# Kernel tuning notes

Hardware: AMD Instinct MI355X
Metric: run time of the kernel (lower is better)

The kernel has to match this reference:

```python
import jax, jax.numpy as jnp
import numpy as np

K_DIM = 256
HEADS = 8


def setup_inputs() -> dict:
    key = jax.random.key(0)
    ks = jax.random.split(key, 6)
    b, t, k, h = 8, 1024, K_DIM, HEADS
    scale = 1.0 / np.sqrt(k)
    x = jax.random.normal(ks[0], (b, t, k), dtype=jnp.float32)
    # nn.Linear(k, k*h, bias=False) weights, stored as (in, out) for x @ W
    Wq = jax.random.normal(ks[1], (k, k * h), dtype=jnp.float32) * scale
    Wk = jax.random.normal(ks[2], (k, k * h), dtype=jnp.float32) * scale
    Wv = jax.random.normal(ks[3], (k, k * h), dtype=jnp.float32) * scale
    # unifyheads: nn.Linear(h*k, k) with bias
    Wu = jax.random.normal(ks[4], (h * k, k), dtype=jnp.float32) * (1.0 / np.sqrt(h * k))
    bu = jax.random.normal(ks[5], (k,), dtype=jnp.float32) * 0.01
    return {"x": x, "Wq": Wq, "Wk": Wk, "Wv": Wv, "Wu": Wu, "bu": bu}


def reference(x, Wq, Wk, Wv, Wu, bu):
    b, t, k = x.shape
    h = Wq.shape[1] // k
    inv4 = 1.0 / (k ** 0.25)  # scale Q and K each by k^(1/4) -> combined 1/sqrt(k)
    q = (x @ Wq).reshape(b, t, h, k) * inv4
    kk = (x @ Wk).reshape(b, t, h, k) * inv4
    v = (x @ Wv).reshape(b, t, h, k)
    # scores: [b, h, t, t]
    scores = jnp.einsum('bthk,bshk->bhts', q, kk)
    att = jax.nn.softmax(scores, axis=-1)
    out = jnp.einsum('bhts,bshk->bthk', att, v).reshape(b, t, h * k)
    return out @ Wu + bu
```

## Files before the change

kernel.cpp:

```cpp
#include <hip/hip_runtime.h>
#include <stdint.h>

typedef unsigned short u16;
typedef __attribute__((ext_vector_type(8))) short bf16x8;
typedef __attribute__((ext_vector_type(4))) float f32x4;

#define LOG2E 1.44269504088896340736f

__device__ __forceinline__ float bf2f(u16 u) {
  union { uint32_t u; float f; } v; v.u = ((uint32_t)u) << 16; return v.f;
}
__device__ __forceinline__ u16 f2bf(float f) {
  union { float f; uint32_t u; } v; v.f = f;
  uint32_t r = v.u + 0x7fffu + ((v.u >> 16) & 1u);
  return (u16)(r >> 16);
}

__device__ __forceinline__ void gl_lds16(const u16* g, u16* l) {
  __builtin_amdgcn_global_load_lds((const __attribute__((address_space(1))) void*)g,
                                   (__attribute__((address_space(3))) void*)l, 16, 0, 0);
}

__global__ __launch_bounds__(256) void k_cvt_x(const float* __restrict__ x,
                                               u16* __restrict__ xb) {
  const int i = blockIdx.x * 256 + threadIdx.x;
  float4 v = ((const float4*)x)[i];
  ushort4 o;
  o.x = f2bf(v.x); o.y = f2bf(v.y); o.z = f2bf(v.z); o.w = f2bf(v.w);
  ((ushort4*)xb)[i] = o;
}

__device__ __forceinline__ void transpose64f(const float* src, int sstride,
                                             u16* dst, int dstride,
                                             float scale, u16* tile ) {
  const int tid = threadIdx.x;
  const int row = tid >> 3, seg = tid & 7;
#pragma unroll
  for (int p = 0; p < 2; ++p) {
    int rr = p * 32 + row;
    int rw = rr ^ (seg * 8);
    float4 a = *(const float4*)(src + rr * sstride + seg * 8);
    float4 b = *(const float4*)(src + rr * sstride + seg * 8 + 4);
    tile[(seg * 8 + 0) * 80 + rw] = f2bf(a.x * scale);
    tile[(seg * 8 + 1) * 80 + rw] = f2bf(a.y * scale);
    tile[(seg * 8 + 2) * 80 + rw] = f2bf(a.z * scale);
    tile[(seg * 8 + 3) * 80 + rw] = f2bf(a.w * scale);
    tile[(seg * 8 + 4) * 80 + rw] = f2bf(b.x * scale);
    tile[(seg * 8 + 5) * 80 + rw] = f2bf(b.y * scale);
    tile[(seg * 8 + 6) * 80 + rw] = f2bf(b.z * scale);
    tile[(seg * 8 + 7) * 80 + rw] = f2bf(b.w * scale);
  }
  __syncthreads();
#pragma unroll
  for (int p = 0; p < 2; ++p) {
    int rr = p * 32 + row;
    int sw = (seg ^ ((rr >> 3) & 7)) * 8;
    *(uint4*)(dst + rr * dstride + seg * 8) = *(uint4*)(tile + rr * 80 + sw);
  }
}

__device__ __forceinline__ void transpose64(const u16* src, int sstride,
                                            u16* dst, int dstride, u16* tile) {
  const int tid = threadIdx.x;
  const int row = tid >> 3, seg = tid & 7;
  union { uint4 u; u16 s[8]; } tv;
#pragma unroll
  for (int p = 0; p < 2; ++p) {
    int rr = p * 32 + row;
    int rw = rr ^ (seg * 8);
    tv.u = *(const uint4*)(src + rr * sstride + seg * 8);
#pragma unroll
    for (int j = 0; j < 8; ++j)
      tile[(seg * 8 + j) * 80 + rw] = tv.s[j];
  }
  __syncthreads();
#pragma unroll
  for (int p = 0; p < 2; ++p) {
    int rr = p * 32 + row;
    int sw = (seg ^ ((rr >> 3) & 7)) * 8;
    *(uint4*)(dst + rr * dstride + seg * 8) = *(uint4*)(tile + rr * 80 + sw);
  }
}

__global__ __launch_bounds__(256) void k_transpose_wqkv(const float* __restrict__ Wq,
                                                        const float* __restrict__ Wk,
                                                        const float* __restrict__ Wv,
                                                        u16* __restrict__ Wt) {
  __shared__ u16 tile[64 * 80];
  const int o0 = blockIdx.x * 64, i0 = blockIdx.y * 64;
  const float* src; float scale = 0.25f; int oc0 = o0;
  if (o0 < 2048)      { src = Wq; }
  else if (o0 < 4096) { src = Wk; oc0 = o0 - 2048; }
  else                { src = Wv; oc0 = o0 - 4096; scale = 1.0f; }
  transpose64f(src + i0 * 2048 + oc0, 2048, Wt + o0 * 256 + i0, 256, scale, tile);
}

__global__ __launch_bounds__(256) void k_transpose_wu(const float* __restrict__ Wu,
                                                      u16* __restrict__ Wut) {
  __shared__ u16 tile[64 * 80];
  const int c0 = blockIdx.x * 64, r0 = blockIdx.y * 64;
  transpose64f(Wu + r0 * 256 + c0, 256, Wut + c0 * 2048 + r0, 2048, 1.0f, tile);
}

__global__ __launch_bounds__(256) void k_transpose_v(const u16* __restrict__ qkv,
                                                     u16* __restrict__ vt) {
  __shared__ u16 tile[64 * 80];
  const int bh = blockIdx.z;
  const int b = bh >> 3, h = bh & 7;
  const int t0 = blockIdx.y * 64, d0 = blockIdx.x * 64;
  const u16* src = qkv + ((size_t)(b * 1024 + t0)) * 6144 + 4096 + h * 256 + d0;
  u16* dst = vt + ((size_t)(bh * 256 + d0)) * 1024 + t0;
  transpose64(src, 6144, dst, 1024, tile);
}

__global__ __launch_bounds__(256) void k_gemm_qkv(const u16* __restrict__ A,
                                                  const u16* __restrict__ Bt,
                                                  u16* __restrict__ C) {
  __shared__ u16 As[128 * 32];
  __shared__ u16 Bs[128 * 32];
  const int m0 = blockIdx.y * 128, n0 = blockIdx.x * 128;
  const int tid = threadIdx.x, w = tid >> 6, lane = tid & 63;
  const int q = lane >> 4, r = lane & 15;
  const int wm = (w >> 1) * 64, wn = (w & 1) * 64;
  const int bo0 = w * 2048 + lane * 16;
  const int row0 = bo0 >> 6, col0 = (bo0 & 63) >> 1;
  const int bo1 = bo0 + 1024;
  const int row1 = bo1 >> 6, col1 = (bo1 & 63) >> 1;
  f32x4 acc[4][4] = {};
  for (int kt = 0; kt < 256; kt += 32) {
    __syncthreads();
    gl_lds16(A + (m0 + row0) * 256 + kt + col0, As + w * 1024);
    gl_lds16(A + (m0 + row1) * 256 + kt + col1, As + w * 1024 + 512);
    gl_lds16(Bt + (n0 + row0) * 256 + kt + col0, Bs + w * 1024);
    gl_lds16(Bt + (n0 + row1) * 256 + kt + col1, Bs + w * 1024 + 512);
    __syncthreads();
    bf16x8 af[4], bf[4];
#pragma unroll
    for (int mb = 0; mb < 4; ++mb) af[mb] = *(const bf16x8*)(As + (wm + mb * 16 + r) * 32 + q * 8);
#pragma unroll
    for (int nb = 0; nb < 4; ++nb) bf[nb] = *(const bf16x8*)(Bs + (wn + nb * 16 + r) * 32 + q * 8);
#pragma unroll
    for (int mb = 0; mb < 4; ++mb)
#pragma unroll
      for (int nb = 0; nb < 4; ++nb)
        acc[mb][nb] = __builtin_amdgcn_mfma_f32_16x16x32_bf16(af[mb], bf[nb], acc[mb][nb], 0, 0, 0);
  }
#pragma unroll
  for (int mb = 0; mb < 4; ++mb)
#pragma unroll
    for (int nb = 0; nb < 4; ++nb) {
      const int nn = n0 + wn + nb * 16 + r;
#pragma unroll
      for (int reg = 0; reg < 4; ++reg) {
        const int mm = m0 + wm + mb * 16 + q * 4 + reg;
        C[(size_t)mm * 6144 + nn] = f2bf(acc[mb][nb][reg]);
      }
    }
}

__global__ __launch_bounds__(256, 2) void k_attn(const u16* __restrict__ qkv,
                                                 const u16* __restrict__ vt,
                                                 u16* __restrict__ att) {
  __shared__ u16 smem[17152];
  const int blk = blockIdx.x;
  const int qt = blk >> 6, bh = blk & 63;
  const int b = bh >> 3, h = bh & 7;
  const int tid = threadIdx.x, w = tid >> 6, lane = tid & 63;
  const int q = lane >> 4, r = lane & 15;
  const int t0 = qt * 128 + w * 32;

  const u16* QgA = qkv + ((size_t)(b * 1024 + t0 + r)) * 6144 + h * 256;
  const u16* QgB = QgA + (size_t)16 * 6144;
  bf16x8 qfA[8], qfB[8];
#pragma unroll
  for (int kc = 0; kc < 8; ++kc) {
    qfA[kc] = *(const bf16x8*)(QgA + kc * 32 + q * 8);
    qfB[kc] = *(const bf16x8*)(QgB + kc * 32 + q * 8);
  }

  float lA = 0.0f, lB = 0.0f;
  f32x4 oA[16] = {}, oB[16] = {};

  const u16* Kg = qkv + (size_t)b * 1024 * 6144 + 2048 + h * 256;
  const u16* Vg = vt + (size_t)(b * 8 + h) * 256 * 1024;

  const int kc_s = (tid & 31) >> 2, kq_s = tid & 3;
  const int db_s = tid >> 4, vr_s = tid & 15;

  for (int sc = 0; sc < 1024; sc += 32) {
    __syncthreads();
    {
      uint4 kv[4];
#pragma unroll
      for (int p = 0; p < 4; ++p) {
        int key = p * 8 + (tid >> 5);
        kv[p] = *(const uint4*)(Kg + (size_t)(sc + key) * 6144 + (tid & 31) * 8);
      }
#pragma unroll
      for (int p = 0; p < 4; ++p) {
        int key = p * 8 + (tid >> 5);
        int sb = key >> 4, kr = key & 15;
        int unit = (kc_s * 2 + sb) * 64 + kq_s * 16 + ((kr + kq_s + kc_s * 4) & 15);
        *(uint4*)(smem + unit * 8) = kv[p];
      }
    }
    {
      uint4 vv[4];
#pragma unroll
      for (int p = 0; p < 4; ++p)
        vv[p] = *(const uint4*)(Vg + (size_t)tid * 1024 + sc + p * 8);
#pragma unroll
      for (int p = 0; p < 4; ++p) {
        int unit = db_s * 64 + p * 16 + ((vr_s + p) & 15);
        *(uint4*)(smem + 8192 + unit * 8) = vv[p];
      }
    }
    __syncthreads();

    f32x4 s0A = {}, s1A = {}, s0B = {}, s1B = {};
#pragma unroll
    for (int kc = 0; kc < 8; ++kc) {
      bf16x8 k0 = *(const bf16x8*)(smem + ((kc * 2 + 0) * 64 + q * 16 + ((r + q + kc * 4) & 15)) * 8);
      bf16x8 k1 = *(const bf16x8*)(smem + ((kc * 2 + 1) * 64 + q * 16 + ((r + q + kc * 4) & 15)) * 8);
      s0A = __builtin_amdgcn_mfma_f32_16x16x32_bf16(k0, qfA[kc], s0A, 0, 0, 0);
      s1A = __builtin_amdgcn_mfma_f32_16x16x32_bf16(k1, qfA[kc], s1A, 0, 0, 0);
      s0B = __builtin_amdgcn_mfma_f32_16x16x32_bf16(k0, qfB[kc], s0B, 0, 0, 0);
      s1B = __builtin_amdgcn_mfma_f32_16x16x32_bf16(k1, qfB[kc], s1B, 0, 0, 0);
    }

    union { bf16x8 v; u16 e[8]; } pfA, pfB;
    {
      float pa[4], pb[4];
#pragma unroll
      for (int reg = 0; reg < 4; ++reg) {
        pa[reg] = exp2f(s0A[reg] * LOG2E);
        pb[reg] = exp2f(s1A[reg] * LOG2E);
        lA += pa[reg] + pb[reg];
      }
      uint32_t pk[4];
#pragma unroll
      for (int reg = 0; reg < 4; ++reg)
        pk[reg] = (uint32_t)f2bf(pa[reg]) | ((uint32_t)f2bf(pb[reg]) << 16);
      const int srcA = ((q & 1) << 5) + r, srcB = srcA + 16;
      uint32_t tt[8];
#pragma unroll
      for (int reg = 0; reg < 4; ++reg) tt[reg] = (uint32_t)__shfl((int)pk[reg], srcA);
#pragma unroll
      for (int reg = 0; reg < 4; ++reg) tt[4 + reg] = (uint32_t)__shfl((int)pk[reg], srcB);
      const bool hi = (q >= 2);
#pragma unroll
      for (int j = 0; j < 8; ++j)
        pfA.e[j] = hi ? (u16)(tt[j] >> 16) : (u16)(tt[j] & 0xffffu);
    }
    {
      float pa[4], pb[4];
#pragma unroll
      for (int reg = 0; reg < 4; ++reg) {
        pa[reg] = exp2f(s0B[reg] * LOG2E);
        pb[reg] = exp2f(s1B[reg] * LOG2E);
        lB += pa[reg] + pb[reg];
      }
      uint32_t pk[4];
#pragma unroll
      for (int reg = 0; reg < 4; ++reg)
        pk[reg] = (uint32_t)f2bf(pa[reg]) | ((uint32_t)f2bf(pb[reg]) << 16);
      const int srcA = ((q & 1) << 5) + r, srcB = srcA + 16;
      uint32_t tt[8];
#pragma unroll
      for (int reg = 0; reg < 4; ++reg) tt[reg] = (uint32_t)__shfl((int)pk[reg], srcA);
#pragma unroll
      for (int reg = 0; reg < 4; ++reg) tt[4 + reg] = (uint32_t)__shfl((int)pk[reg], srcB);
      const bool hi = (q >= 2);
#pragma unroll
      for (int j = 0; j < 8; ++j)
        pfB.e[j] = hi ? (u16)(tt[j] >> 16) : (u16)(tt[j] & 0xffffu);
    }

#pragma unroll
    for (int db = 0; db < 16; ++db) {
      bf16x8 vf = *(const bf16x8*)(smem + 8192 + (db * 64 + q * 16 + ((r + q) & 15)) * 8);
      oA[db] = __builtin_amdgcn_mfma_f32_16x16x32_bf16(vf, pfA.v, oA[db], 0, 0, 0);
      oB[db] = __builtin_amdgcn_mfma_f32_16x16x32_bf16(vf, pfB.v, oB[db], 0, 0, 0);
    }
  }

  lA += __shfl_xor(lA, 16); lA += __shfl_xor(lA, 32);
  lB += __shfl_xor(lB, 16); lB += __shfl_xor(lB, 32);
  float rlA = 1.0f / lA, rlB = 1.0f / lB;

  __syncthreads();
  u16* Os = smem + w * 4288;
#pragma unroll
  for (int pass = 0; pass < 2; ++pass) {
    const f32x4* o = pass ? oB : oA;
    const float rl = pass ? rlB : rlA;
    const int tb = t0 + pass * 16;
    __syncthreads();
#pragma unroll
    for (int db = 0; db < 16; ++db) {
      uint32_t lo = (uint32_t)f2bf(o[db][0] * rl) | ((uint32_t)f2bf(o[db][1] * rl) << 16);
      uint32_t hi2 = (uint32_t)f2bf(o[db][2] * rl) | ((uint32_t)f2bf(o[db][3] * rl) << 16);
      uint2 val; val.x = lo; val.y = hi2;
      *(uint2*)(Os + r * 268 + db * 16 + q * 4) = val;
    }
    asm volatile("s_waitcnt lgkmcnt(0)" ::: "memory");
    u16* Ag = att + ((size_t)(b * 1024 + tb)) * 2048 + h * 256;
#pragma unroll
    for (int p = 0; p < 8; ++p) {
      int idx = (p * 64 + lane) * 8;
      int row = idx >> 8, col = idx & 255;
      *(uint4*)(Ag + (size_t)row * 2048 + col) = *(uint4*)(Os + row * 268 + col);
    }
  }
}

__global__ __launch_bounds__(256) void k_gemm_out(const u16* __restrict__ A,
                                                  const u16* __restrict__ Bt,
                                                  const float* __restrict__ bu,
                                                  float* __restrict__ C) {
  __shared__ u16 As[128 * 32];
  __shared__ u16 Bs[64 * 32];
  const int m0 = blockIdx.y * 128, n0 = blockIdx.x * 64;
  const int tid = threadIdx.x, w = tid >> 6, lane = tid & 63;
  const int q = lane >> 4, r = lane & 15;
  const int wm = (w >> 1) * 64, wn = (w & 1) * 32;
  const int boA0 = w * 2048 + lane * 16;
  const int rA0 = boA0 >> 6, cA0 = (boA0 & 63) >> 1;
  const int boA1 = boA0 + 1024;
  const int rA1 = boA1 >> 6, cA1 = (boA1 & 63) >> 1;
  const int boB = w * 1024 + lane * 16;
  const int rB = boB >> 6, cB = (boB & 63) >> 1;
  f32x4 acc[4][2] = {};
  for (int kt = 0; kt < 2048; kt += 32) {
    __syncthreads();
    gl_lds16(A + (size_t)(m0 + rA0) * 2048 + kt + cA0, As + w * 1024);
    gl_lds16(A + (size_t)(m0 + rA1) * 2048 + kt + cA1, As + w * 1024 + 512);
    gl_lds16(Bt + (size_t)(n0 + rB) * 2048 + kt + cB, Bs + w * 512);
    __syncthreads();
    bf16x8 af[4], bf[2];
#pragma unroll
    for (int mb = 0; mb < 4; ++mb) af[mb] = *(const bf16x8*)(As + (wm + mb * 16 + r) * 32 + q * 8);
#pragma unroll
    for (int nb = 0; nb < 2; ++nb) bf[nb] = *(const bf16x8*)(Bs + (wn + nb * 16 + r) * 32 + q * 8);
#pragma unroll
    for (int mb = 0; mb < 4; ++mb)
#pragma unroll
      for (int nb = 0; nb < 2; ++nb)
        acc[mb][nb] = __builtin_amdgcn_mfma_f32_16x16x32_bf16(af[mb], bf[nb], acc[mb][nb], 0, 0, 0);
  }
  float bias[2];
#pragma unroll
  for (int nb = 0; nb < 2; ++nb) bias[nb] = bu[n0 + wn + nb * 16 + r];
#pragma unroll
  for (int mb = 0; mb < 4; ++mb)
#pragma unroll
    for (int nb = 0; nb < 2; ++nb) {
      const int nn = n0 + wn + nb * 16 + r;
#pragma unroll
      for (int reg = 0; reg < 4; ++reg) {
        const int mm = m0 + wm + mb * 16 + q * 4 + reg;
        C[(size_t)mm * 256 + nn] = acc[mb][nb][reg] + bias[nb];
      }
    }
}

extern "C" void kernel_launch(void* const* d_in, const int* in_sizes, int n_in,
                              void* d_out, int out_size, void* d_ws, size_t ws_size,
                              hipStream_t stream) {
  const float* x  = (const float*)d_in[0];
  const float* Wq = (const float*)d_in[1];
  const float* Wk = (const float*)d_in[2];
  const float* Wv = (const float*)d_in[3];
  const float* Wu = (const float*)d_in[4];
  const float* bu = (const float*)d_in[5];
  float* outp = (float*)d_out;

  char* ws = (char*)d_ws;
  u16* qkv   = (u16*)(ws);
  u16* vt    = (u16*)(ws + 100663296);
  u16* attb  = (u16*)(ws + 134217728);
  u16* wqkvt = (u16*)(ws + 167772160);
  u16* wut   = (u16*)(ws + 170917888);
  u16* xb    = (u16*)(ws + 171966464);
  (void)in_sizes; (void)n_in; (void)out_size; (void)ws_size;

  dim3 blk(256);
  k_cvt_x<<<dim3(2048), blk, 0, stream>>>(x, xb);
  k_transpose_wqkv<<<dim3(96, 4), blk, 0, stream>>>(Wq, Wk, Wv, wqkvt);
  k_transpose_wu<<<dim3(4, 32), blk, 0, stream>>>(Wu, wut);
  k_gemm_qkv<<<dim3(48, 64), blk, 0, stream>>>(xb, wqkvt, qkv);
  k_transpose_v<<<dim3(4, 16, 64), blk, 0, stream>>>(qkv, vt);
  k_attn<<<dim3(512), blk, 0, stream>>>(qkv, vt, attb);
  k_gemm_out<<<dim3(4, 64), blk, 0, stream>>>(attb, wut, bu, outp);
}
```

Before: 272.7 us.

## Fuse V transpose into QKV GEMM, prefetch K/V in attention, retile output GEMM

The QKV GEMM epilogue now writes V tiles directly in transposed layout, which removes the separate V transpose kernel and its extra pass over memory. The attention loop register-prefetches the next K/V chunk while the current one is being computed, so global load latency can overlap with MFMA work. The output GEMM moves to 64x64 tiles, doubling the block count to 512 for better CU occupancy at the cost of more redundant B loads. Together these touch three separate kernels.

```diff
diff --git a/kernel.cpp b/kernel.cpp
--- a/kernel.cpp
+++ b/kernel.cpp
@@ -59,29 +59,6 @@
   }
 }
 
-__device__ __forceinline__ void transpose64(const u16* src, int sstride,
-                                            u16* dst, int dstride, u16* tile) {
-  const int tid = threadIdx.x;
-  const int row = tid >> 3, seg = tid & 7;
-  union { uint4 u; u16 s[8]; } tv;
-#pragma unroll
-  for (int p = 0; p < 2; ++p) {
-    int rr = p * 32 + row;
-    int rw = rr ^ (seg * 8);
-    tv.u = *(const uint4*)(src + rr * sstride + seg * 8);
-#pragma unroll
-    for (int j = 0; j < 8; ++j)
-      tile[(seg * 8 + j) * 80 + rw] = tv.s[j];
-  }
-  __syncthreads();
-#pragma unroll
-  for (int p = 0; p < 2; ++p) {
-    int rr = p * 32 + row;
-    int sw = (seg ^ ((rr >> 3) & 7)) * 8;
-    *(uint4*)(dst + rr * dstride + seg * 8) = *(uint4*)(tile + rr * 80 + sw);
-  }
-}
-
 __global__ __launch_bounds__(256) void k_transpose_wqkv(const float* __restrict__ Wq,
                                                         const float* __restrict__ Wk,
                                                         const float* __restrict__ Wv,
@@ -102,20 +79,10 @@
   transpose64f(Wu + r0 * 256 + c0, 256, Wut + c0 * 2048 + r0, 2048, 1.0f, tile);
 }
 
-__global__ __launch_bounds__(256) void k_transpose_v(const u16* __restrict__ qkv,
-                                                     u16* __restrict__ vt) {
-  __shared__ u16 tile[64 * 80];
-  const int bh = blockIdx.z;
-  const int b = bh >> 3, h = bh & 7;
-  const int t0 = blockIdx.y * 64, d0 = blockIdx.x * 64;
-  const u16* src = qkv + ((size_t)(b * 1024 + t0)) * 6144 + 4096 + h * 256 + d0;
-  u16* dst = vt + ((size_t)(bh * 256 + d0)) * 1024 + t0;
-  transpose64(src, 6144, dst, 1024, tile);
-}
-
 __global__ __launch_bounds__(256) void k_gemm_qkv(const u16* __restrict__ A,
                                                   const u16* __restrict__ Bt,
-                                                  u16* __restrict__ C) {
+                                                  u16* __restrict__ C,
+                                                  u16* __restrict__ vt) {
   __shared__ u16 As[128 * 32];
   __shared__ u16 Bs[128 * 32];
   const int m0 = blockIdx.y * 128, n0 = blockIdx.x * 128;
@@ -145,17 +112,32 @@
       for (int nb = 0; nb < 4; ++nb)
         acc[mb][nb] = __builtin_amdgcn_mfma_f32_16x16x32_bf16(af[mb], bf[nb], acc[mb][nb], 0, 0, 0);
   }
-#pragma unroll
-  for (int mb = 0; mb < 4; ++mb)
-#pragma unroll
-    for (int nb = 0; nb < 4; ++nb) {
-      const int nn = n0 + wn + nb * 16 + r;
-#pragma unroll
-      for (int reg = 0; reg < 4; ++reg) {
-        const int mm = m0 + wm + mb * 16 + q * 4 + reg;
-        C[(size_t)mm * 6144 + nn] = f2bf(acc[mb][nb][reg]);
-      }
-    }
+  if (n0 < 4096) {
+#pragma unroll
+    for (int mb = 0; mb < 4; ++mb)
+#pragma unroll
+      for (int nb = 0; nb < 4; ++nb) {
+        const int nn = n0 + wn + nb * 16 + r;
+#pragma unroll
+        for (int reg = 0; reg < 4; ++reg) {
+          const int mm = m0 + wm + mb * 16 + q * 4 + reg;
+          C[(size_t)mm * 6144 + nn] = f2bf(acc[mb][nb][reg]);
+        }
+      }
+  } else {
+#pragma unroll
+    for (int mb = 0; mb < 4; ++mb)
+#pragma unroll
+      for (int nb = 0; nb < 4; ++nb) {
+        const int hd = n0 - 4096 + wn + nb * 16 + r;
+        const int mm0 = m0 + wm + mb * 16 + q * 4;
+        const int bb = mm0 >> 10, t = mm0 & 1023;
+        uint2 val;
+        val.x = (uint32_t)f2bf(acc[mb][nb][0]) | ((uint32_t)f2bf(acc[mb][nb][1]) << 16);
+        val.y = (uint32_t)f2bf(acc[mb][nb][2]) | ((uint32_t)f2bf(acc[mb][nb][3]) << 16);
+        *(uint2*)(vt + ((size_t)(bb * 2048 + hd)) * 1024 + t) = val;
+      }
+  }
 }
 
 __global__ __launch_bounds__(256, 2) void k_attn(const u16* __restrict__ qkv,
@@ -187,35 +169,38 @@
   const int kc_s = (tid & 31) >> 2, kq_s = tid & 3;
   const int db_s = tid >> 4, vr_s = tid & 15;
 
+  uint4 kpre[4], vpre[4];
+#pragma unroll
+  for (int p = 0; p < 4; ++p) {
+    int key = p * 8 + (tid >> 5);
+    kpre[p] = *(const uint4*)(Kg + (size_t)key * 6144 + (tid & 31) * 8);
+    vpre[p] = *(const uint4*)(Vg + (size_t)tid * 1024 + p * 8);
+  }
+
   for (int sc = 0; sc < 1024; sc += 32) {
     __syncthreads();
-    {
-      uint4 kv[4];
+#pragma unroll
+    for (int p = 0; p < 4; ++p) {
+      int key = p * 8 + (tid >> 5);
+      int sb = key >> 4, kr = key & 15;
+      int unit = (kc_s * 2 + sb) * 64 + kq_s * 16 + ((kr + kq_s + kc_s * 4) & 15);
+      *(uint4*)(smem + unit * 8) = kpre[p];
+    }
+#pragma unroll
+    for (int p = 0; p < 4; ++p) {
+      int unit = db_s * 64 + p * 16 + ((vr_s + p) & 15);
+      *(uint4*)(smem + 8192 + unit * 8) = vpre[p];
+    }
+    __syncthreads();
+
+    if (sc + 32 < 1024) {
 #pragma unroll
       for (int p = 0; p < 4; ++p) {
         int key = p * 8 + (tid >> 5);
-        kv[p] = *(const uint4*)(Kg + (size_t)(sc + key) * 6144 + (tid & 31) * 8);
-      }
-#pragma unroll
-      for (int p = 0; p < 4; ++p) {
-        int key = p * 8 + (tid >> 5);
-        int sb = key >> 4, kr = key & 15;
-        int unit = (kc_s * 2 + sb) * 64 + kq_s * 16 + ((kr + kq_s + kc_s * 4) & 15);
-        *(uint4*)(smem + unit * 8) = kv[p];
-      }
-    }
-    {
-      uint4 vv[4];
-#pragma unroll
-      for (int p = 0; p < 4; ++p)
-        vv[p] = *(const uint4*)(Vg + (size_t)tid * 1024 + sc + p * 8);
-#pragma unroll
-      for (int p = 0; p < 4; ++p) {
-        int unit = db_s * 64 + p * 16 + ((vr_s + p) & 15);
-        *(uint4*)(smem + 8192 + unit * 8) = vv[p];
-      }
-    }
-    __syncthreads();
+        kpre[p] = *(const uint4*)(Kg + (size_t)(sc + 32 + key) * 6144 + (tid & 31) * 8);
+        vpre[p] = *(const uint4*)(Vg + (size_t)tid * 1024 + sc + 32 + p * 8);
+      }
+    }
 
     f32x4 s0A = {}, s1A = {}, s0B = {}, s1B = {};
 #pragma unroll
@@ -318,32 +303,27 @@
                                                   const u16* __restrict__ Bt,
                                                   const float* __restrict__ bu,
                                                   float* __restrict__ C) {
-  __shared__ u16 As[128 * 32];
+  __shared__ u16 As[64 * 32];
   __shared__ u16 Bs[64 * 32];
-  const int m0 = blockIdx.y * 128, n0 = blockIdx.x * 64;
+  const int m0 = blockIdx.y * 64, n0 = blockIdx.x * 64;
   const int tid = threadIdx.x, w = tid >> 6, lane = tid & 63;
   const int q = lane >> 4, r = lane & 15;
-  const int wm = (w >> 1) * 64, wn = (w & 1) * 32;
-  const int boA0 = w * 2048 + lane * 16;
-  const int rA0 = boA0 >> 6, cA0 = (boA0 & 63) >> 1;
-  const int boA1 = boA0 + 1024;
-  const int rA1 = boA1 >> 6, cA1 = (boA1 & 63) >> 1;
-  const int boB = w * 1024 + lane * 16;
-  const int rB = boB >> 6, cB = (boB & 63) >> 1;
-  f32x4 acc[4][2] = {};
+  const int wm = (w >> 1) * 32, wn = (w & 1) * 32;
+  const int bo = w * 1024 + lane * 16;
+  const int rw = bo >> 6, cl = (bo & 63) >> 1;
+  f32x4 acc[2][2] = {};
   for (int kt = 0; kt < 2048; kt += 32) {
     __syncthreads();
-    gl_lds16(A + (size_t)(m0 + rA0) * 2048 + kt + cA0, As + w * 1024);
-    gl_lds16(A + (size_t)(m0 + rA1) * 2048 + kt + cA1, As + w * 1024 + 512);
-    gl_lds16(Bt + (size_t)(n0 + rB) * 2048 + kt + cB, Bs + w * 512);
-    __syncthreads();
-    bf16x8 af[4], bf[2];
-#pragma unroll
-    for (int mb = 0; mb < 4; ++mb) af[mb] = *(const bf16x8*)(As + (wm + mb * 16 + r) * 32 + q * 8);
+    gl_lds16(A + (size_t)(m0 + rw) * 2048 + kt + cl, As + w * 512);
+    gl_lds16(Bt + (size_t)(n0 + rw) * 2048 + kt + cl, Bs + w * 512);
+    __syncthreads();
+    bf16x8 af[2], bf[2];
+#pragma unroll
+    for (int mb = 0; mb < 2; ++mb) af[mb] = *(const bf16x8*)(As + (wm + mb * 16 + r) * 32 + q * 8);
 #pragma unroll
     for (int nb = 0; nb < 2; ++nb) bf[nb] = *(const bf16x8*)(Bs + (wn + nb * 16 + r) * 32 + q * 8);
 #pragma unroll
-    for (int mb = 0; mb < 4; ++mb)
+    for (int mb = 0; mb < 2; ++mb)
 #pragma unroll
       for (int nb = 0; nb < 2; ++nb)
         acc[mb][nb] = __builtin_amdgcn_mfma_f32_16x16x32_bf16(af[mb], bf[nb], acc[mb][nb], 0, 0, 0);
@@ -352,7 +332,7 @@
 #pragma unroll
   for (int nb = 0; nb < 2; ++nb) bias[nb] = bu[n0 + wn + nb * 16 + r];
 #pragma unroll
-  for (int mb = 0; mb < 4; ++mb)
+  for (int mb = 0; mb < 2; ++mb)
 #pragma unroll
     for (int nb = 0; nb < 2; ++nb) {
       const int nn = n0 + wn + nb * 16 + r;
@@ -388,8 +368,7 @@
   k_cvt_x<<<dim3(2048), blk, 0, stream>>>(x, xb);
   k_transpose_wqkv<<<dim3(96, 4), blk, 0, stream>>>(Wq, Wk, Wv, wqkvt);
   k_transpose_wu<<<dim3(4, 32), blk, 0, stream>>>(Wu, wut);
-  k_gemm_qkv<<<dim3(48, 64), blk, 0, stream>>>(xb, wqkvt, qkv);
-  k_transpose_v<<<dim3(4, 16, 64), blk, 0, stream>>>(qkv, vt);
+  k_gemm_qkv<<<dim3(48, 64), blk, 0, stream>>>(xb, wqkvt, qkv, vt);
   k_attn<<<dim3(512), blk, 0, stream>>>(qkv, vt, attb);
-  k_gemm_out<<<dim3(4, 64), blk, 0, stream>>>(attb, wut, bu, outp);
-}
+  k_gemm_out<<<dim3(4, 128), blk, 0, stream>>>(attb, wut, bu, outp);
+}
```

Result: slower. 396.8 us (+45.5%).
